# Kernel tuning notes

Measured on AMD Instinct MI355X. Metric: run time of the kernel, lower is better.

## Reference

```python
import jax, jax.numpy as jnp
import numpy as np

B, S, F, H = 64, 100, 128, 8
D = F // H
SCALE = D ** -0.5


def setup_inputs() -> dict:
    key = jax.random.key(0)
    ks = jax.random.split(key, 12)
    def lin(k, fan_in, fan_out):
        bound = 1.0 / np.sqrt(fan_in)
        kw, kb = jax.random.split(k)
        W = jax.random.uniform(kw, (fan_in, fan_out), minval=-bound, maxval=bound, dtype=jnp.float32)
        b = jax.random.uniform(kb, (fan_out,), minval=-bound, maxval=bound, dtype=jnp.float32)
        return W, b
    Wq, bq = lin(ks[0], F, F)
    Wk, bk = lin(ks[1], F, F)
    Wv, bv = lin(ks[2], F, F)
    Wo, bo = lin(ks[3], F, F)
    q = jax.random.normal(ks[4], (B, S, F), dtype=jnp.float32)
    k = jax.random.normal(ks[5], (B, S, F), dtype=jnp.float32)
    v = jax.random.normal(ks[6], (B, S, F), dtype=jnp.float32)
    # causal mask broadcast over heads: 1 = keep, 0 = masked
    mask = jnp.tril(jnp.ones((S, S), dtype=jnp.float32))[None, None, :, :].repeat(B, axis=0)
    return {"q": q, "k": k, "v": v, "mask": mask,
            "Wq": Wq, "bq": bq, "Wk": Wk, "bk": bk,
            "Wv": Wv, "bv": bv, "Wo": Wo, "bo": bo}


def reference(q, k, v, mask, Wq, bq, Wk, bk, Wv, bv, Wo, bo):
    # project and split heads: [B,S,F] -> [B,H,S,D]
    def heads(x, W, b):
        y = x @ W + b
        return y.reshape(B, S, H, D).transpose(0, 2, 1, 3)
    qh = heads(q, Wq, bq)
    kh = heads(k, Wk, bk)
    vh = heads(v, Wv, bv)
    scores = jnp.einsum('bhqd,bhkd->bhqk', qh, kh) * SCALE
    scores = jnp.where(mask == 0, -1e9, scores)
    attn = jax.nn.softmax(scores, axis=-1)
    out = jnp.einsum('bhqk,bhkd->bhqd', attn, vh)
    out = out.transpose(0, 2, 1, 3).reshape(B, S, F)
    return out @ Wo + bo
```

## Files before the change

kernel.cpp:

```cpp
#include <hip/hip_runtime.h>
#include <hip/hip_bf16.h>

typedef __attribute__((ext_vector_type(8))) short bf16x8;
typedef __attribute__((ext_vector_type(4))) float f32x4;

#define Bb 64
#define Ss 100
#define Ff 128
#define Hh 8
#define ROWS (Bb * Ss)
#define ELEMS (ROWS * Ff)

__device__ __forceinline__ unsigned short f2bf(float f) {
    unsigned u = __float_as_uint(f);
    u += 0x7FFFu + ((u >> 16) & 1u);
    return (unsigned short)(u >> 16);
}

__device__ __forceinline__ bf16x8 load_a8(const float* p) {
    float4 x0 = *(const float4*)p;
    float4 x1 = *(const float4*)(p + 4);
    bf16x8 a;
    a[0] = (short)f2bf(x0.x); a[1] = (short)f2bf(x0.y);
    a[2] = (short)f2bf(x0.z); a[3] = (short)f2bf(x0.w);
    a[4] = (short)f2bf(x1.x); a[5] = (short)f2bf(x1.y);
    a[6] = (short)f2bf(x1.z); a[7] = (short)f2bf(x1.w);
    return a;
}

__global__ __launch_bounds__(448) void fused_qkv_attn_kernel(
    const float* __restrict__ q, const float* __restrict__ k, const float* __restrict__ v,
    const float* __restrict__ Wq, const float* __restrict__ bq,
    const float* __restrict__ Wk, const float* __restrict__ bk,
    const float* __restrict__ Wv, const float* __restrict__ bv,
    const float* __restrict__ Wo,
    unsigned short* __restrict__ ao, unsigned short* __restrict__ WtO)
{
    const int blk = blockIdx.x;
    const int t = threadIdx.x;

    if (blk >= Bb * Hh) {
        if (t < 256) {
            const int kb = blk - Bb * Hh;
            const int n  = t >> 1;
            const int k0 = kb * 16 + (t & 1) * 8;
            bf16x8 vv;
#pragma unroll
            for (int j = 0; j < 8; ++j) vv[j] = (short)f2bf(Wo[(k0 + j) * Ff + n]);
            *(bf16x8*)&WtO[n * Ff + k0] = vv;
        }
        return;
    }

    __shared__ unsigned short lds[32896];
    const int b = blk >> 3, h = blk & 7;

    {
        int4* z = (int4*)&lds[6528];
        for (int i = t; i < 3296; i += 448) z[i] = make_int4(0, 0, 0, 0);
    }
    for (int i = t; i < 3 * 2048; i += 448) {
        const int p = i >> 11, rem = i & 2047;
        const int kk = rem >> 4, n = rem & 15;
        const float* Wp = p == 0 ? Wq : p == 1 ? Wk : Wv;
        lds[p * 2176 + n * 136 + kk] = f2bf(Wp[kk * Ff + h * 16 + n]);
    }
    __syncthreads();

    const int w = t >> 6, lane = t & 63, m = lane & 15, g = lane >> 4;
    f32x4 zz = {0.f, 0.f, 0.f, 0.f};

    const int rowb = w * 16 + m;
    const int rowc = rowb < Ss ? rowb : Ss - 1;
    const float* xq = q + (b * Ss + rowc) * Ff + g * 8;
    const float* xk = k + (b * Ss + rowc) * Ff + g * 8;
    const float* xv = v + (b * Ss + rowc) * Ff + g * 8;

    f32x4 accq = zz, acck = zz, accv = zz;
#pragma unroll
    for (int kk = 0; kk < 4; ++kk) {
        const int xo = kk * 32;
        const int wo = m * 136 + kk * 32 + g * 8;
        bf16x8 bqf = *(const bf16x8*)&lds[wo];
        bf16x8 bkf = *(const bf16x8*)&lds[2176 + wo];
        bf16x8 bvf = *(const bf16x8*)&lds[4352 + wo];
        accq = __builtin_amdgcn_mfma_f32_16x16x32_bf16(load_a8(xq + xo), bqf, accq, 0, 0, 0);
        acck = __builtin_amdgcn_mfma_f32_16x16x32_bf16(load_a8(xk + xo), bkf, acck, 0, 0, 0);
        accv = __builtin_amdgcn_mfma_f32_16x16x32_bf16(load_a8(xv + xo), bvf, accv, 0, 0, 0);
    }
    {
        const float bbq = bq[h * 16 + m];
        const float bbk = bk[h * 16 + m];
        const float bbv = bv[h * 16 + m];
#pragma unroll
        for (int r = 0; r < 4; ++r) {
            const int row = w * 16 + g * 4 + r;
            lds[6528  + row * 40 + m]  = f2bf(accq[r] + bbq);
            lds[11008 + row * 40 + m]  = f2bf(acck[r] + bbk);
            lds[15488 + m * 136 + row] = f2bf(accv[r] + bbv);
        }
    }
    __syncthreads();

    bf16x8 aq = *(const bf16x8*)&lds[6528 + (w * 16 + m) * 40 + g * 8];
    f32x4 sc[7];
#pragma unroll
    for (int tt = 0; tt < 7; ++tt) {
        bf16x8 bkf = *(const bf16x8*)&lds[11008 + (tt * 16 + m) * 40 + g * 8];
        sc[tt] = __builtin_amdgcn_mfma_f32_16x16x32_bf16(aq, bkf, zz, 0, 0, 0);
    }

    const int rbase = w * 16 + g * 4;
    float mx[4], sum[4], invl[4];
#pragma unroll
    for (int r = 0; r < 4; ++r) mx[r] = -3.0e38f;
#pragma unroll
    for (int tt = 0; tt < 7; ++tt)
#pragma unroll
        for (int r = 0; r < 4; ++r) {
            float sv = (tt * 16 + m <= rbase + r) ? sc[tt][r] * 0.25f : -1.0e30f;
            sc[tt][r] = sv;
            mx[r] = fmaxf(mx[r], sv);
        }
#pragma unroll
    for (int off = 1; off < 16; off <<= 1)
#pragma unroll
        for (int r = 0; r < 4; ++r) mx[r] = fmaxf(mx[r], __shfl_xor(mx[r], off));
#pragma unroll
    for (int r = 0; r < 4; ++r) sum[r] = 0.f;

    unsigned short* Pw = &lds[17664 + w * 2176];
#pragma unroll
    for (int tt = 0; tt < 7; ++tt)
#pragma unroll
        for (int r = 0; r < 4; ++r) {
            float e = __expf(sc[tt][r] - mx[r]);
            sum[r] += e;
            Pw[(g * 4 + r) * 136 + tt * 16 + m] = f2bf(e);
        }
#pragma unroll
    for (int off = 1; off < 16; off <<= 1)
#pragma unroll
        for (int r = 0; r < 4; ++r) sum[r] += __shfl_xor(sum[r], off);
#pragma unroll
    for (int r = 0; r < 4; ++r) invl[r] = 1.0f / sum[r];

    f32x4 oacc = zz;
#pragma unroll
    for (int kk = 0; kk < 128; kk += 32) {
        bf16x8 ap = *(const bf16x8*)&Pw[m * 136 + kk + g * 8];
        bf16x8 bvf = *(const bf16x8*)&lds[15488 + m * 136 + kk + g * 8];
        oacc = __builtin_amdgcn_mfma_f32_16x16x32_bf16(ap, bvf, oacc, 0, 0, 0);
    }
#pragma unroll
    for (int r = 0; r < 4; ++r) {
        const int s = rbase + r;
        if (s < Ss)
            ao[(b * Ss + s) * Ff + h * 16 + m] = f2bf(oacc[r] * invl[r]);
    }
}

__global__ __launch_bounds__(256) void proj_out_kernel(
    const unsigned short* __restrict__ ao, const unsigned short* __restrict__ WtO,
    const float* __restrict__ bo, float* __restrict__ out)
{
    __shared__ unsigned short Xs[64 * 136];
    __shared__ unsigned short Ws[128 * 136];
    const int t = threadIdx.x;
    const int r0 = blockIdx.x * 64;
#pragma unroll
    for (int i = 0; i < 4; ++i) {
        int idx = t + i * 256;
        int r = idx >> 4, c8 = (idx & 15) * 8;
        *(bf16x8*)&Xs[r * 136 + c8] = *(const bf16x8*)&ao[(r0 + r) * Ff + c8];
    }
#pragma unroll
    for (int i = 0; i < 8; ++i) {
        int r = (t >> 4) + i * 16, c8 = (t & 15) * 8;
        *(bf16x8*)&Ws[r * 136 + c8] = *(const bf16x8*)&WtO[r * Ff + c8];
    }
    __syncthreads();

    const int w = t >> 6, lane = t & 63, m = lane & 15, g = lane >> 4;
    f32x4 zz = {0.f, 0.f, 0.f, 0.f};
    f32x4 acc[8];
#pragma unroll
    for (int n = 0; n < 8; ++n) acc[n] = zz;
#pragma unroll
    for (int kk = 0; kk < 128; kk += 32) {
        bf16x8 a = *(const bf16x8*)&Xs[(w * 16 + m) * 136 + kk + g * 8];
#pragma unroll
        for (int n = 0; n < 8; ++n) {
            bf16x8 bf = *(const bf16x8*)&Ws[(n * 16 + m) * 136 + kk + g * 8];
            acc[n] = __builtin_amdgcn_mfma_f32_16x16x32_bf16(a, bf, acc[n], 0, 0, 0);
        }
    }

#pragma unroll
    for (int n = 0; n < 8; ++n) {
        float bb = bo[n * 16 + m];
#pragma unroll
        for (int r = 0; r < 4; ++r) {
            int row = r0 + w * 16 + g * 4 + r;
            out[row * Ff + n * 16 + m] = acc[n][r] + bb;
        }
    }
}

extern "C" void kernel_launch(void* const* d_in, const int* in_sizes, int n_in,
                              void* d_out, int out_size, void* d_ws, size_t ws_size,
                              hipStream_t stream) {
    const float* q  = (const float*)d_in[0];
    const float* k  = (const float*)d_in[1];
    const float* v  = (const float*)d_in[2];
    const float* Wq = (const float*)d_in[4];
    const float* bq = (const float*)d_in[5];
    const float* Wk = (const float*)d_in[6];
    const float* bk = (const float*)d_in[7];
    const float* Wv = (const float*)d_in[8];
    const float* bv = (const float*)d_in[9];
    const float* Wo = (const float*)d_in[10];
    const float* bo = (const float*)d_in[11];

    float* out = (float*)d_out;
    unsigned short* wsu = (unsigned short*)d_ws;
    unsigned short* WtO = wsu;
    unsigned short* ao  = wsu + 16384;

    fused_qkv_attn_kernel<<<dim3(Bb * Hh + 8), dim3(448), 0, stream>>>(
        q, k, v, Wq, bq, Wk, bk, Wv, bv, Wo, ao, WtO);
    proj_out_kernel<<<dim3(100), dim3(256), 0, stream>>>(ao, WtO, bo, out);
}
```

Measured before the change: 101.7 us.

## Shrink LDS by aliasing P buffer over weights; vectorize weight staging and zeroing

Shared memory use drops from about 64KB to 35KB by reusing the QKV weight region for the per-wave softmax P tiles once projections are done, with an extra barrier to guard the reuse. Weight loads now read float4 from global instead of scalars, and only the padding regions that must be zero are cleared instead of the whole buffer. Launch bounds add a minimum-blocks hint to allow more resident workgroups per CU, which may constrain register allocation.

```diff
diff --git a/kernel.cpp b/kernel.cpp
--- a/kernel.cpp
+++ b/kernel.cpp
@@ -3,13 +3,12 @@
 
 typedef __attribute__((ext_vector_type(8))) short bf16x8;
 typedef __attribute__((ext_vector_type(4))) float f32x4;
+typedef __attribute__((ext_vector_type(4))) unsigned short us4;
 
 #define Bb 64
 #define Ss 100
 #define Ff 128
 #define Hh 8
-#define ROWS (Bb * Ss)
-#define ELEMS (ROWS * Ff)
 
 __device__ __forceinline__ unsigned short f2bf(float f) {
     unsigned u = __float_as_uint(f);
@@ -28,7 +27,7 @@
     return a;
 }
 
-__global__ __launch_bounds__(448) void fused_qkv_attn_kernel(
+__global__ __launch_bounds__(448, 6) void fused_qkv_attn_kernel(
     const float* __restrict__ q, const float* __restrict__ k, const float* __restrict__ v,
     const float* __restrict__ Wq, const float* __restrict__ bq,
     const float* __restrict__ Wk, const float* __restrict__ bk,
@@ -52,18 +51,31 @@
         return;
     }
 
-    __shared__ unsigned short lds[32896];
+    __shared__ unsigned short lds[17664];
     const int b = blk >> 3, h = blk & 7;
 
+    for (int i = t; i < 1536; i += 448) {
+        const int p = i >> 9, rem = i & 511;
+        const int kk = rem >> 2, n4 = (rem & 3) * 4;
+        const float* Wp = p == 0 ? Wq : p == 1 ? Wk : Wv;
+        const float4 wv = *(const float4*)&Wp[kk * Ff + h * 16 + n4];
+        lds[p * 2176 + (n4 + 0) * 136 + kk] = f2bf(wv.x);
+        lds[p * 2176 + (n4 + 1) * 136 + kk] = f2bf(wv.y);
+        lds[p * 2176 + (n4 + 2) * 136 + kk] = f2bf(wv.z);
+        lds[p * 2176 + (n4 + 3) * 136 + kk] = f2bf(wv.w);
+    }
     {
-        int4* z = (int4*)&lds[6528];
-        for (int i = t; i < 3296; i += 448) z[i] = make_int4(0, 0, 0, 0);
-    }
-    for (int i = t; i < 3 * 2048; i += 448) {
-        const int p = i >> 11, rem = i & 2047;
-        const int kk = rem >> 4, n = rem & 15;
-        const float* Wp = p == 0 ? Wq : p == 1 ? Wk : Wv;
-        lds[p * 2176 + n * 136 + kk] = f2bf(Wp[kk * Ff + h * 16 + n]);
+        const us4 z4 = {0, 0, 0, 0};
+        for (int i = t; i < 1008; i += 448) {
+            if (i < 896) {
+                const int row = i >> 3, rem = i & 7;
+                const int base = (rem >> 2) ? 11008 : 6528;
+                *(us4*)&lds[base + row * 40 + 16 + (rem & 3) * 4] = z4;
+            } else {
+                const int j = i - 896;
+                *(us4*)&lds[15488 + (j / 7) * 136 + 100 + (j % 7) * 4] = z4;
+            }
+        }
     }
     __syncthreads();
 
@@ -126,10 +138,16 @@
     for (int off = 1; off < 16; off <<= 1)
 #pragma unroll
         for (int r = 0; r < 4; ++r) mx[r] = fmaxf(mx[r], __shfl_xor(mx[r], off));
+
+    __syncthreads();
+
+    unsigned short* Pw = &lds[w * 2176];
+    {
+        const us4 z4 = {0, 0, 0, 0};
+        *(us4*)&Pw[m * 136 + 112 + g * 4] = z4;
+    }
 #pragma unroll
     for (int r = 0; r < 4; ++r) sum[r] = 0.f;
-
-    unsigned short* Pw = &lds[17664 + w * 2176];
 #pragma unroll
     for (int tt = 0; tt < 7; ++tt)
 #pragma unroll
@@ -148,7 +166,7 @@
     f32x4 oacc = zz;
 #pragma unroll
     for (int kk = 0; kk < 128; kk += 32) {
-        bf16x8 ap = *(const bf16x8*)&Pw[m * 136 + kk + g * 8];
+        bf16x8 ap  = *(const bf16x8*)&Pw[m * 136 + kk + g * 8];
         bf16x8 bvf = *(const bf16x8*)&lds[15488 + m * 136 + kk + g * 8];
         oacc = __builtin_amdgcn_mfma_f32_16x16x32_bf16(ap, bvf, oacc, 0, 0, 0);
     }
```

After: 98.78 us. 1.03x faster.
